# Optimization experiments

Measured on AMD Instinct MI355X. Metric: run time of the kernel, lower is better.

The kernel has to match this reference:

```python
import jax, jax.numpy as jnp
import numpy as np

NPOINT = 2048
K = 16
EPS = 1e-5


def farthest_point_sample(xyz, npoint):
    # xyz: (B, N, 3) -> (B, npoint) int32 indices. Deterministic start at index 0.
    B, N, _ = xyz.shape
    batch = jnp.arange(B)

    def step(carry, _):
        dists, far = carry                      # (B,N), (B,)
        centroid = xyz[batch, far]              # (B,3)
        d = jnp.sum((xyz - centroid[:, None, :]) ** 2, axis=-1)  # (B,N)
        dists = jnp.minimum(dists, d)
        nxt = jnp.argmax(dists, axis=-1).astype(jnp.int32)
        return (dists, nxt), far

    init = (jnp.full((B, N), 1e10, xyz.dtype), jnp.zeros((B,), jnp.int32))
    _, idx = jax.lax.scan(step, init, None, length=npoint)
    return jnp.transpose(idx)                   # (B, npoint)


def knn_query(k, xyz, query_xyz):
    # squared-distance KNN via matmul form (same ordering as torch.cdist+topk smallest)
    x2 = jnp.sum(xyz * xyz, axis=-1)            # (B,N)
    q2 = jnp.sum(query_xyz * query_xyz, axis=-1)  # (B,S)
    sqd = q2[:, :, None] + x2[:, None, :] - 2.0 * jnp.einsum('bsd,bnd->bsn', query_xyz, xyz)
    _, idx = jax.lax.top_k(-sqd, k)             # smallest k distances
    return idx                                  # (B,S,k)


def layer_norm(x, g, b):
    mu = jnp.mean(x, axis=-1, keepdims=True)
    var = jnp.mean((x - mu) ** 2, axis=-1, keepdims=True)
    return (x - mu) * jax.lax.rsqrt(var + EPS) * g + b


def setup_inputs() -> dict:
    key = jax.random.key(0)
    ks = jax.random.split(key, 6)
    B, N, IN_DIM, OUT_DIM = 4, 8192, 64, 128
    C_IN = 3 + IN_DIM
    s1 = 1.0 / np.sqrt(C_IN)
    s2 = 1.0 / np.sqrt(OUT_DIM)
    return {
        'xyz': jax.random.normal(ks[0], (B, N, 3), jnp.float32),
        'feat': jax.random.normal(ks[1], (B, N, IN_DIM), jnp.float32),
        'W1': jax.random.uniform(ks[2], (C_IN, OUT_DIM), jnp.float32, -s1, s1),
        'b1': jax.random.uniform(ks[3], (OUT_DIM,), jnp.float32, -s1, s1),
        'W2': jax.random.uniform(ks[4], (OUT_DIM, OUT_DIM), jnp.float32, -s2, s2),
        'b2': jax.random.uniform(ks[5], (OUT_DIM,), jnp.float32, -s2, s2),
        'ln_g': jnp.ones((OUT_DIM,), jnp.float32),
        'ln_b': jnp.zeros((OUT_DIM,), jnp.float32),
    }


def reference(xyz, feat, W1, b1, W2, b2, ln_g, ln_b):
    B = xyz.shape[0]
    bidx = jnp.arange(B)[:, None, None]

    fps_idx = farthest_point_sample(xyz, NPOINT)                 # (B,S)
    new_xyz = jnp.take_along_axis(xyz, fps_idx[:, :, None], axis=1)  # (B,S,3)
    knn_idx = knn_query(K, xyz, new_xyz)                         # (B,S,K)

    grp_xyz = xyz[bidx, knn_idx] - new_xyz[:, :, None, :]        # (B,S,K,3)
    grp_feat = feat[bidx, knn_idx]                               # (B,S,K,in_dim)
    grouped = jnp.concatenate([grp_xyz, grp_feat], axis=-1)      # (B,S,K,3+in_dim)

    h = jax.nn.relu(grouped @ W1 + b1)
    h = h @ W2 + b2                                              # (B,S,K,out_dim)
    new_feat = jnp.max(h, axis=2)                                # (B,S,out_dim)
    return new_xyz, layer_norm(new_feat, ln_g, ln_b)
```

## Files before the change

### kernel.cpp

```cpp
#include <hip/hip_runtime.h>
#include <stdint.h>

#define BB 4
#define NN 8192
#define SS 2048
#define KK 16
#define IND 64
#define CIN 67
#define OD 128

typedef unsigned int   u32;
typedef unsigned long long u64;
typedef float f2 __attribute__((ext_vector_type(2)));

__global__ __launch_bounds__(256) void k_prep(const float* __restrict__ xyz,
                                              float4* __restrict__ pts){
  int i = blockIdx.x * 256 + threadIdx.x;
  if (i >= BB*NN) return;
  float x = xyz[3*i+0];
  float y = xyz[3*i+1];
  float z = xyz[3*i+2];
  float x2 = __fadd_rn(__fadd_rn(__fmul_rn(x,x), __fmul_rn(y,y)), __fmul_rn(z,z));
  pts[i] = make_float4(x,y,z,x2);
}

template<int CTRL>
__device__ __forceinline__ float dpp_mv(float x){
  int xi = __builtin_bit_cast(int, x);
  int r  = __builtin_amdgcn_update_dpp(xi, xi, CTRL, 0xf, 0xf, false);
  return __builtin_bit_cast(float, r);
}

#define FPT 512
#define PPT (NN/FPT)
#define NW  (FPT/64)
#define FPS_LDS ((3*NN + 3*SS)*4)
__global__ __launch_bounds__(FPT) void k_fps(const float4* __restrict__ pts,
                                             float* __restrict__ out_xyz){
  #pragma clang fp contract(off)
  extern __shared__ float smem[];
  float* sx = smem;
  float* sy = smem +   NN;
  float* sz = smem + 2*NN;
  float* rx = smem + 3*NN;
  float* ry = smem + 3*NN +   SS;
  float* rz = smem + 3*NN + 2*SS;
  __shared__ u64 pkey[2][NW];
  int b = blockIdx.x;
  int tid = threadIdx.x;
  int wid = tid >> 6, lane = tid & 63;
  const float4* P = pts + (size_t)b*NN;
  f2 X[PPT/2], Y[PPT/2], Z[PPT/2], D[PPT/2];
  #pragma unroll
  for (int jp=0;jp<PPT/2;jp++){
    int n0 = tid*PPT + 2*jp;
    float4 p0 = P[n0];
    float4 p1 = P[n0+1];
    X[jp] = (f2){p0.x, p1.x};
    Y[jp] = (f2){p0.y, p1.y};
    Z[jp] = (f2){p0.z, p1.z};
    D[jp] = (f2){1e10f, 1e10f};
    sx[n0]=p0.x; sx[n0+1]=p1.x;
    sy[n0]=p0.y; sy[n0+1]=p1.y;
    sz[n0]=p0.z; sz[n0+1]=p1.z;
  }
  float4 p0v = P[0];
  float cx=p0v.x, cy=p0v.y, cz=p0v.z;
  if (tid==0){ rx[0]=cx; ry[0]=cy; rz[0]=cz; }
  __syncthreads();

  for (int it=1; it<SS; ++it){
    f2 mm = (f2){-1.0f, -1.0f};
    #pragma unroll
    for (int jp=0;jp<PPT/2;jp++){
      f2 dx = X[jp] - cx;
      f2 dy = Y[jp] - cy;
      f2 dz = Z[jp] - cz;
      f2 d  = ((dx*dx) + (dy*dy)) + (dz*dz);
      f2 nd = __builtin_elementwise_min(D[jp], d);
      D[jp] = nd;
      mm = __builtin_elementwise_max(mm, nd);
    }
    float md = fmaxf(mm.x, mm.y);
    float m = md;
    m = fmaxf(m, dpp_mv<0x111>(m));
    m = fmaxf(m, dpp_mv<0x112>(m));
    m = fmaxf(m, dpp_mv<0x114>(m));
    m = fmaxf(m, dpp_mv<0x118>(m));
    m = fmaxf(m, dpp_mv<0x142>(m));
    m = fmaxf(m, dpp_mv<0x143>(m));
    float wmax = __builtin_bit_cast(float,
        __builtin_amdgcn_readlane(__builtin_bit_cast(int, m), 63));
    u64 ball = __ballot(md == wmax);
    int wl = __ffsll((unsigned long long)ball) - 1;
    int bj = 0;
    if (md == wmax){
      #pragma unroll
      for (int t=PPT-1;t>=0;--t){
        float v = (t&1)? D[t>>1].y : D[t>>1].x;
        if (v == wmax) bj = t;
      }
    }
    int widx = __shfl(tid*PPT + bj, wl, 64);
    if (lane==0){
      pkey[it&1][wid] = ((u64)__float_as_uint(wmax) << 32) | (u32)~(u32)widx;
    }
    __syncthreads();
    u64 bk = pkey[it&1][0];
    #pragma unroll
    for (int w=1;w<NW;w++){
      u64 k2 = pkey[it&1][w];
      if (k2 > bk) bk = k2;
    }
    int gw = (int)~(u32)bk;
    cx = sx[gw]; cy = sy[gw]; cz = sz[gw];
    if (tid==0){ rx[it]=cx; ry[it]=cy; rz[it]=cz; }
  }
  __syncthreads();
  for (int i=tid; i<SS; i+=FPT){
    size_t o = (size_t)b*SS*3 + (size_t)i*3;
    out_xyz[o]=rx[i]; out_xyz[o+1]=ry[i]; out_xyz[o+2]=rz[i];
  }
}

__global__ __launch_bounds__(256) void k_knn_mlp(const float4* __restrict__ pts,
                                                 const float* __restrict__ ctr,
                                                 const float* __restrict__ feat,
                                                 const float* __restrict__ W1, const float* __restrict__ b1,
                                                 const float* __restrict__ W2, const float* __restrict__ b2,
                                                 const float* __restrict__ g_ln, const float* __restrict__ b_ln,
                                                 float* __restrict__ out_feat){
  __shared__ float gbuf[4][CIN][16];
  __shared__ float hbuf[4][OD][20];
  int wid = threadIdx.x>>6, lane = threadIdx.x&63;
  int q = blockIdx.x*4 + wid;
  int b = q / SS;
  const float4* P = pts + (size_t)b*NN;
  float qx=ctr[3*q], qy=ctr[3*q+1], qz=ctr[3*q+2];
  float q2 = __fadd_rn(__fadd_rn(__fmul_rn(qx,qx),__fmul_rn(qy,qy)),__fmul_rn(qz,qz));
  u64 key[KK];
  #pragma unroll
  for (int t=0;t<KK;t++) key[t] = ~0ull;
  for (int i=0;i<NN/64;i++){
    int n = i*64 + lane;
    float4 p = P[n];
    float dot = __fadd_rn(__fadd_rn(__fmul_rn(qx,p.x),__fmul_rn(qy,p.y)),__fmul_rn(qz,p.z));
    float sd  = __fsub_rn(__fadd_rn(q2,p.w), __fmul_rn(2.0f,dot));
    u32 bu = __float_as_uint(sd);
    bu ^= (u32)((int)bu >> 31) | 0x80000000u;
    u64 kk = ((u64)bu<<32) | (u32)n;
    if (kk < key[KK-1]){
      key[KK-1] = kk;
      #pragma unroll
      for (int t=KK-1;t>0;--t){
        u64 a=key[t-1], c=key[t];
        bool sw = c < a;
        key[t-1] = sw? c : a;
        key[t]   = sw? a : c;
      }
    }
  }
  int k = lane & 15, part = lane >> 4;
  int n_sel = 0;
  #pragma unroll 1
  for (int r=0;r<KK;r++){
    u64 m = key[0];
    #pragma unroll
    for (int mm=1;mm<64;mm<<=1){
      u64 om = __shfl_xor((unsigned long long)m, mm, 64);
      if (om < m) m = om;
    }
    if (k == r) n_sel = (int)(u32)m;
    if (key[0]==m){
      #pragma unroll
      for (int t=0;t<KK-1;t++) key[t]=key[t+1];
      key[KK-1]=~0ull;
    }
  }
  float* gw = &gbuf[wid][0][0];
  float* hw = &hbuf[wid][0][0];
  {
    const float* fp = feat + ((size_t)b*NN + (size_t)n_sel)*IND + part*16;
    float4 f0 = *(const float4*)(fp+0);
    float4 f1 = *(const float4*)(fp+4);
    float4 f2v = *(const float4*)(fp+8);
    float4 f3 = *(const float4*)(fp+12);
    float v[16] = {f0.x,f0.y,f0.z,f0.w, f1.x,f1.y,f1.z,f1.w,
                   f2v.x,f2v.y,f2v.z,f2v.w, f3.x,f3.y,f3.z,f3.w};
    #pragma unroll
    for (int c=0;c<16;c++) gw[(3+part*16+c)*16 + k] = v[c];
    if (part==0){
      float4 p = P[n_sel];
      gw[0*16+k] = __fsub_rn(p.x, qx);
      gw[1*16+k] = __fsub_rn(p.y, qy);
      gw[2*16+k] = __fsub_rn(p.z, qz);
    }
  }
  __syncthreads();
  int o = lane;
  float a0[16], a1[16];
  #pragma unroll
  for (int t=0;t<16;t++){ a0[t]=0.0f; a1[t]=0.0f; }
  #pragma unroll 4
  for (int j=0;j<CIN;j++){
    float w0 = W1[j*OD + o];
    float w1 = W1[j*OD + o + 64];
    #pragma unroll
    for (int t=0;t<16;t++){
      float gv = gw[j*16+t];
      a0[t]=fmaf(gv,w0,a0[t]); a1[t]=fmaf(gv,w1,a1[t]);
    }
  }
  float bb0 = b1[o], bb1 = b1[o+64];
  #pragma unroll
  for (int t=0;t<16;t++){
    hw[o*20+t]      = fmaxf(a0[t]+bb0, 0.0f);
    hw[(o+64)*20+t] = fmaxf(a1[t]+bb1, 0.0f);
  }
  __syncthreads();
  float c0[16], c1[16];
  #pragma unroll
  for (int t=0;t<16;t++){ c0[t]=0.0f; c1[t]=0.0f; }
  #pragma unroll 4
  for (int j=0;j<OD;j++){
    float w0 = W2[j*OD + o];
    float w1 = W2[j*OD + o + 64];
    #pragma unroll
    for (int t=0;t<16;t++){
      float hv = hw[j*20+t];
      c0[t]=fmaf(hv,w0,c0[t]); c1[t]=fmaf(hv,w1,c1[t]);
    }
  }
  float m0=c0[0], m1=c1[0];
  #pragma unroll
  for (int t=1;t<16;t++){ m0=fmaxf(m0,c0[t]); m1=fmaxf(m1,c1[t]); }
  m0 += b2[o]; m1 += b2[o+64];
  float ssum = m0+m1;
  #pragma unroll
  for (int mm=1;mm<64;mm<<=1) ssum += __shfl_xor(ssum,mm,64);
  float mean = ssum * (1.0f/128.0f);
  float d0=m0-mean, d1=m1-mean;
  float sq = d0*d0 + d1*d1;
  #pragma unroll
  for (int mm=1;mm<64;mm<<=1) sq += __shfl_xor(sq,mm,64);
  float var = sq * (1.0f/128.0f);
  float x = var + 1e-5f;
  float r = rsqrtf(x);
  r = r * (1.5f - 0.5f*x*r*r);
  size_t obf = (size_t)q*OD;
  out_feat[obf+o]    = fmaf(d0*r, g_ln[o],    b_ln[o]);
  out_feat[obf+o+64] = fmaf(d1*r, g_ln[o+64], b_ln[o+64]);
}

extern "C" void kernel_launch(void* const* d_in, const int* in_sizes, int n_in,
                              void* d_out, int out_size, void* d_ws, size_t ws_size,
                              hipStream_t stream){
  const float* xyz  = (const float*)d_in[0];
  const float* feat = (const float*)d_in[1];
  const float* W1   = (const float*)d_in[2];
  const float* b1   = (const float*)d_in[3];
  const float* W2   = (const float*)d_in[4];
  const float* b2   = (const float*)d_in[5];
  const float* lg   = (const float*)d_in[6];
  const float* lb   = (const float*)d_in[7];
  float* out = (float*)d_out;
  float4* pts = (float4*)d_ws;
  float* out_xyz  = out;
  float* out_feat = out + (size_t)BB*SS*3;

  hipFuncSetAttribute((const void*)k_fps,
                      hipFuncAttributeMaxDynamicSharedMemorySize, FPS_LDS);

  hipLaunchKernelGGL(k_prep,    dim3((BB*NN+255)/256), dim3(256), 0,       stream, xyz, pts);
  hipLaunchKernelGGL(k_fps,     dim3(BB),              dim3(FPT), FPS_LDS, stream, pts, out_xyz);
  hipLaunchKernelGGL(k_knn_mlp, dim3(BB*SS/4),         dim3(256), 0,       stream,
                     pts, out_xyz, feat, W1, b1, W2, b2, lg, lb, out_feat);
}
```

Measured before the change: 2.498 ms.

## Split fused KNN+MLP kernel into separate KNN and MLP kernels

Splits the fused KNN selection and MLP kernel into two kernels that communicate through a workspace buffer of neighbor indices. The KNN kernel no longer carries the MLP's register and LDS footprint, so more waves can be resident to hide the latency of its distance scan. The MLP kernel reloads the indices and centers from global memory. It also adds a min-blocks hint of 2 to the FPS kernel's launch bounds. The cost is one extra launch and a small global write and read of indices.

```diff
diff --git a/kernel.cpp b/kernel.cpp
--- a/kernel.cpp
+++ b/kernel.cpp
@@ -35,8 +35,8 @@
 #define PPT (NN/FPT)
 #define NW  (FPT/64)
 #define FPS_LDS ((3*NN + 3*SS)*4)
-__global__ __launch_bounds__(FPT) void k_fps(const float4* __restrict__ pts,
-                                             float* __restrict__ out_xyz){
+__global__ __launch_bounds__(FPT, 2) void k_fps(const float4* __restrict__ pts,
+                                                float* __restrict__ out_xyz){
   #pragma clang fp contract(off)
   extern __shared__ float smem[];
   float* sx = smem;
@@ -123,17 +123,11 @@
   }
 }
 
-__global__ __launch_bounds__(256) void k_knn_mlp(const float4* __restrict__ pts,
-                                                 const float* __restrict__ ctr,
-                                                 const float* __restrict__ feat,
-                                                 const float* __restrict__ W1, const float* __restrict__ b1,
-                                                 const float* __restrict__ W2, const float* __restrict__ b2,
-                                                 const float* __restrict__ g_ln, const float* __restrict__ b_ln,
-                                                 float* __restrict__ out_feat){
-  __shared__ float gbuf[4][CIN][16];
-  __shared__ float hbuf[4][OD][20];
-  int wid = threadIdx.x>>6, lane = threadIdx.x&63;
-  int q = blockIdx.x*4 + wid;
+__global__ __launch_bounds__(256) void k_knn(const float4* __restrict__ pts,
+                                             const float* __restrict__ ctr,
+                                             int* __restrict__ knn_idx){
+  int q = blockIdx.x*4 + (threadIdx.x>>6);
+  int lane = threadIdx.x & 63;
   int b = q / SS;
   const float4* P = pts + (size_t)b*NN;
   float qx=ctr[3*q], qy=ctr[3*q+1], qz=ctr[3*q+2];
@@ -160,8 +154,6 @@
       }
     }
   }
-  int k = lane & 15, part = lane >> 4;
-  int n_sel = 0;
   #pragma unroll 1
   for (int r=0;r<KK;r++){
     u64 m = key[0];
@@ -170,17 +162,34 @@
       u64 om = __shfl_xor((unsigned long long)m, mm, 64);
       if (om < m) m = om;
     }
-    if (k == r) n_sel = (int)(u32)m;
+    if (lane==0) knn_idx[q*KK + r] = (int)(u32)m;
     if (key[0]==m){
       #pragma unroll
       for (int t=0;t<KK-1;t++) key[t]=key[t+1];
       key[KK-1]=~0ull;
     }
   }
+}
+
+__global__ __launch_bounds__(256) void k_mlp(const float* __restrict__ feat,
+                                             const float4* __restrict__ pts,
+                                             const float* __restrict__ ctr,
+                                             const int* __restrict__ knn_idx,
+                                             const float* __restrict__ W1, const float* __restrict__ b1,
+                                             const float* __restrict__ W2, const float* __restrict__ b2,
+                                             const float* __restrict__ g_ln, const float* __restrict__ b_ln,
+                                             float* __restrict__ out_feat){
+  __shared__ float gbuf[4][CIN][16];
+  __shared__ float hbuf[4][OD][20];
+  int wid = threadIdx.x>>6, lane = threadIdx.x&63;
+  int q = blockIdx.x*4 + wid;
+  int b = q / SS;
   float* gw = &gbuf[wid][0][0];
   float* hw = &hbuf[wid][0][0];
+  int k = lane & 15, part = lane >> 4;
+  int n = knn_idx[q*KK + k];
   {
-    const float* fp = feat + ((size_t)b*NN + (size_t)n_sel)*IND + part*16;
+    const float* fp = feat + ((size_t)b*NN + (size_t)n)*IND + part*16;
     float4 f0 = *(const float4*)(fp+0);
     float4 f1 = *(const float4*)(fp+4);
     float4 f2v = *(const float4*)(fp+8);
@@ -190,10 +199,10 @@
     #pragma unroll
     for (int c=0;c<16;c++) gw[(3+part*16+c)*16 + k] = v[c];
     if (part==0){
-      float4 p = P[n_sel];
-      gw[0*16+k] = __fsub_rn(p.x, qx);
-      gw[1*16+k] = __fsub_rn(p.y, qy);
-      gw[2*16+k] = __fsub_rn(p.z, qz);
+      float4 p = pts[(size_t)b*NN + n];
+      gw[0*16+k] = __fsub_rn(p.x, ctr[3*q+0]);
+      gw[1*16+k] = __fsub_rn(p.y, ctr[3*q+1]);
+      gw[2*16+k] = __fsub_rn(p.z, ctr[3*q+2]);
     }
   }
   __syncthreads();
@@ -264,15 +273,18 @@
   const float* lg   = (const float*)d_in[6];
   const float* lb   = (const float*)d_in[7];
   float* out = (float*)d_out;
-  float4* pts = (float4*)d_ws;
+  char* ws = (char*)d_ws;
+  float4* pts = (float4*)ws;
+  int*    kidx = (int*)(ws + 524288);
   float* out_xyz  = out;
   float* out_feat = out + (size_t)BB*SS*3;
 
   hipFuncSetAttribute((const void*)k_fps,
                       hipFuncAttributeMaxDynamicSharedMemorySize, FPS_LDS);
 
-  hipLaunchKernelGGL(k_prep,    dim3((BB*NN+255)/256), dim3(256), 0,       stream, xyz, pts);
-  hipLaunchKernelGGL(k_fps,     dim3(BB),              dim3(FPT), FPS_LDS, stream, pts, out_xyz);
-  hipLaunchKernelGGL(k_knn_mlp, dim3(BB*SS/4),         dim3(256), 0,       stream,
-                     pts, out_xyz, feat, W1, b1, W2, b2, lg, lb, out_feat);
-}
+  hipLaunchKernelGGL(k_prep, dim3((BB*NN+255)/256), dim3(256), 0,       stream, xyz, pts);
+  hipLaunchKernelGGL(k_fps,  dim3(BB),              dim3(FPT), FPS_LDS, stream, pts, out_xyz);
+  hipLaunchKernelGGL(k_knn,  dim3(BB*SS/4),         dim3(256), 0,       stream, pts, out_xyz, kidx);
+  hipLaunchKernelGGL(k_mlp,  dim3(BB*SS/4),         dim3(256), 0,       stream,
+                     feat, pts, out_xyz, kidx, W1, b1, W2, b2, lg, lb, out_feat);
+}
```

Result: faster. 2.408 ms (-3.6%).
